# Optimization experiments

Hardware: AMD Instinct MI355X
Metric: run time of the kernel (lower is better)

The kernel has to match this reference:

```python
import jax, jax.numpy as jnp
import numpy as np

B, C_IN, L, NCLASS = 256, 6, 512, 10

def setup_inputs() -> dict:
    key = jax.random.key(0)
    ks = jax.random.split(key, 16)
    g = lambda k, shp, s=0.05: jax.random.normal(k, shp, dtype=jnp.float32) * s
    return {
        "x": jax.random.normal(ks[0], (B, C_IN, L), dtype=jnp.float32),
        "conv1_w": g(ks[1], (32, C_IN, 3)),
        "conv1_b": g(ks[2], (32,)),
        "bn1_g": jnp.ones((32,), jnp.float32),
        "bn1_b": jnp.zeros((32,), jnp.float32),
        "bn1_m": g(ks[3], (32,)),
        "bn1_v": jnp.abs(g(ks[4], (32,))) + 1.0,
        "conv2_w": g(ks[5], (64, 32, 3)),
        "conv2_b": g(ks[6], (64,)),
        "bn2_g": jnp.ones((64,), jnp.float32),
        "bn2_b": jnp.zeros((64,), jnp.float32),
        "bn2_m": g(ks[7], (64,)),
        "bn2_v": jnp.abs(g(ks[8], (64,))) + 1.0,
        "wq": g(ks[9], (64, 64)),
        "bq": g(ks[10], (64,)),
        "wk": g(ks[11], (64, 64)),
        "bk": g(ks[12], (64,)),
        "wv": g(ks[13], (64, 64)),
        "bv": g(ks[14], (64,)),
        "fc_w": g(ks[15], (NCLASS, 64)),
        "fc_b": jnp.zeros((NCLASS,), jnp.float32),
    }

def _conv1d(x, w, b):
    # x: [B, C, L], w: [O, C, 3], padding=1 -> same length
    y = jax.lax.conv_general_dilated(
        x, w, window_strides=(1,), padding=[(1, 1)],
        dimension_numbers=("NCH", "OIH", "NCH"))
    return y + b[None, :, None]

def _bn(x, g, b, m, v, eps=1e-5):
    # eval-mode BatchNorm1d over channel dim of [B, C, L]
    inv = g * jax.lax.rsqrt(v + eps)
    return x * inv[None, :, None] + (b - m * inv)[None, :, None]

def reference(x, conv1_w, conv1_b, bn1_g, bn1_b, bn1_m, bn1_v,
              conv2_w, conv2_b, bn2_g, bn2_b, bn2_m, bn2_v,
              wq, bq, wk, bk, wv, bv, fc_w, fc_b):
    h = jax.nn.relu(_bn(_conv1d(x, conv1_w, conv1_b), bn1_g, bn1_b, bn1_m, bn1_v))
    h = jax.nn.relu(_bn(_conv1d(h, conv2_w, conv2_b), bn2_g, bn2_b, bn2_m, bn2_v))
    h = h.transpose(0, 2, 1)                      # [B, L, 64]
    q = h @ wq.T + bq
    k = h @ wk.T + bk
    v = h @ wv.T + bv
    scores = jnp.einsum("bqd,bkd->bqk", q, k) / jnp.sqrt(jnp.float32(64.0))
    attn = jax.nn.softmax(scores, axis=-1)
    out = jnp.einsum("bqk,bkd->bqd", attn, v)     # [B, L, 64]
    pooled = out.mean(axis=1)                     # [B, 64]
    return pooled @ fc_w.T + fc_b                 # [B, n_class]
```

## Files before the change

### kernel.cpp

```cpp
#include <hip/hip_runtime.h>
#include <hip/hip_bf16.h>


#define NB 256
#define LL 512
#define CIN 6
#define NCLASS 10
#define SLAB 8192
#define QSC 0.18033688f

typedef __bf16 bf16x8 __attribute__((ext_vector_type(8)));
typedef float f32x4 __attribute__((ext_vector_type(4)));
typedef unsigned short us4 __attribute__((ext_vector_type(4)));
typedef unsigned short us8 __attribute__((ext_vector_type(8)));
typedef unsigned int u32x4 __attribute__((ext_vector_type(4)));

static __device__ __forceinline__ unsigned short f2b(float f) {
    __bf16 h = (__bf16)f;
    return __builtin_bit_cast(unsigned short, h);
}

__global__ __launch_bounds__(256) void prep_weights(
    const float* __restrict__ w1, const float* __restrict__ cb1,
    const float* __restrict__ g1, const float* __restrict__ be1,
    const float* __restrict__ m1, const float* __restrict__ v1,
    const float* __restrict__ w2, const float* __restrict__ cb2,
    const float* __restrict__ g2, const float* __restrict__ be2,
    const float* __restrict__ m2, const float* __restrict__ v2,
    const float* __restrict__ wq, const float* __restrict__ wk,
    const float* __restrict__ wv,
    unsigned short* __restrict__ w1p, float* __restrict__ b1f,
    unsigned short* __restrict__ w2p, float* __restrict__ b2f,
    unsigned short* __restrict__ wqp, unsigned short* __restrict__ wkp,
    unsigned short* __restrict__ wvp)
{
    const int tt = blockIdx.x * 256 + threadIdx.x;
    for (int idx = tt; idx < 1024; idx += 2048) {
        int c = idx >> 5, k = idx & 31;
        int dl = k >> 3, ci = k & 7;
        float inv = g1[c] * rsqrtf(v1[c] + 1e-5f);
        float val = (dl < 3 && ci < 6) ? w1[c * 18 + ci * 3 + dl] * inv : 0.f;
        w1p[idx] = f2b(val);
    }
    if (tt < 32) {
        float inv = g1[tt] * rsqrtf(v1[tt] + 1e-5f);
        b1f[tt] = be1[tt] + (cb1[tt] - m1[tt]) * inv;
    }
    for (int idx = tt; idx < 2048; idx += 2048) {
        int c2 = idx >> 5, ci = idx & 31;
        float inv = g2[c2] * rsqrtf(v2[c2] + 1e-5f);
        const float* wp = w2 + c2 * 96 + ci * 3;
        w2p[c2 * 96 +      ci] = f2b(wp[0] * inv);
        w2p[c2 * 96 + 32 + ci] = f2b(wp[1] * inv);
        w2p[c2 * 96 + 64 + ci] = f2b(wp[2] * inv);
    }
    if (tt >= 64 && tt < 128) {
        int c2 = tt - 64;
        float inv = g2[c2] * rsqrtf(v2[c2] + 1e-5f);
        b2f[c2] = be2[c2] + (cb2[c2] - m2[c2]) * inv;
    }
    for (int idx = tt; idx < 4096; idx += 2048) {
        int d = idx >> 6, k = idx & 63;
        int kc = k >> 5, quad = (k >> 3) & 3, e = k & 7;
        int ch = kc * 32 + (e >> 2) * 16 + quad * 4 + (e & 3);
        wqp[idx] = f2b(wq[d * 64 + ch] * QSC);
        wkp[idx] = f2b(wk[d * 64 + ch]);
        wvp[idx] = f2b(wv[d * 64 + ch]);
    }
}

__global__ __launch_bounds__(512, 2) void fused_all(
    const float* __restrict__ x,
    const unsigned short* __restrict__ w1p, const float* __restrict__ b1f,
    const unsigned short* __restrict__ w2p, const float* __restrict__ b2f,
    const unsigned short* __restrict__ wqp, const unsigned short* __restrict__ wkp,
    const unsigned short* __restrict__ wvp,
    const float* __restrict__ bq, const float* __restrict__ bk,
    const float* __restrict__ bvp,
    const float* __restrict__ fcw, const float* __restrict__ fcb,
    float* __restrict__ outp)
{
    const int b = blockIdx.x;
    const int t = threadIdx.x;
    const int w = t >> 6, lane = t & 63, quad = lane >> 4, lc = lane & 15;

    __shared__ __align__(16) char smem[16 * SLAB + 8192];
    unsigned short* xstage = (unsigned short*)(smem + 16 * SLAB);
    float* redw   = (float*)(smem + 16 * SLAB) + w * 64;
    float* pooled = (float*)(smem + 16 * SLAB + 4096);

    unsigned short* slab[2] = { (unsigned short*)(smem + (2 * w) * SLAB),
                                (unsigned short*)(smem + (2 * w + 1) * SLAB) };

    {
        us8 pk;
        #pragma unroll
        for (int ci = 0; ci < 6; ci++)
            pk[ci] = f2b(x[((size_t)b * CIN + ci) * LL + t]);
        pk[6] = 0; pk[7] = 0;
        *(us8*)&xstage[t * 8] = pk;
    }
    __syncthreads();

    {
        bf16x8 bW1[2];
        #pragma unroll
        for (int nt = 0; nt < 2; nt++)
            bW1[nt] = *(const bf16x8*)(w1p + (nt * 16 + lc) * 32 + quad * 8);
        f32x4 b1q[2];
        #pragma unroll
        for (int nt = 0; nt < 2; nt++)
            b1q[nt] = *(const f32x4*)&b1f[nt * 16 + quad * 4];
        #pragma unroll
        for (int sg = 0; sg < 2; sg++) {
            const int g = 2 * w + sg;
            unsigned short* h1sl = slab[sg];
            #pragma unroll
            for (int mt = 0; mt < 3; mt++) {
                int j = mt * 16 + lc;
                int P = g * 32 - 1 + j;
                int src = P + quad - 1;
                bool okx = (src >= 0) && (src < LL);
                int srcc = src < 0 ? 0 : (src > 511 ? 511 : src);
                u32x4 xv = *(const u32x4*)&xstage[srcc * 8];
                if (!okx) { xv[0] = 0u; xv[1] = 0u; xv[2] = 0u; xv[3] = 0u; }
                bf16x8 aX = __builtin_bit_cast(bf16x8, xv);
                bool pv = (P >= 0) && (P < LL);
                #pragma unroll
                for (int nt = 0; nt < 2; nt++) {
                    f32x4 z = {0.f, 0.f, 0.f, 0.f};
                    f32x4 h = __builtin_amdgcn_mfma_f32_16x16x32_bf16(bW1[nt], aX, z, 0, 0, 0);
                    us4 pk;
                    #pragma unroll
                    for (int r = 0; r < 4; r++) {
                        float y = h[r] + b1q[nt][r];
                        y = (pv && y > 0.f) ? y : 0.f;
                        pk[r] = f2b(y);
                    }
                    if (j < 34)
                        *(us4*)&h1sl[j * 40 + nt * 16 + quad * 4] = pk;
                }
            }
        }
    }

    bf16x8 bX[2][2][3];
    #pragma unroll
    for (int sg = 0; sg < 2; sg++)
        #pragma unroll
        for (int rt = 0; rt < 2; rt++)
            #pragma unroll
            for (int kc = 0; kc < 3; kc++)
                bX[sg][rt][kc] = *(const bf16x8*)&slab[sg][(rt * 16 + lc + kc) * 40 + quad * 8];

    f32x4 acc2[2][4][2];
    #pragma unroll
    for (int nt = 0; nt < 4; nt++) {
        bf16x8 aW0 = *(const bf16x8*)(w2p + (nt * 16 + lc) * 96 + quad * 8);
        bf16x8 aW1 = *(const bf16x8*)(w2p + (nt * 16 + lc) * 96 + 32 + quad * 8);
        bf16x8 aW2 = *(const bf16x8*)(w2p + (nt * 16 + lc) * 96 + 64 + quad * 8);
        #pragma unroll
        for (int sg = 0; sg < 2; sg++)
            #pragma unroll
            for (int rt = 0; rt < 2; rt++) {
                f32x4 a = {0.f, 0.f, 0.f, 0.f};
                a = __builtin_amdgcn_mfma_f32_16x16x32_bf16(aW0, bX[sg][rt][0], a, 0, 0, 0);
                a = __builtin_amdgcn_mfma_f32_16x16x32_bf16(aW1, bX[sg][rt][1], a, 0, 0, 0);
                acc2[sg][nt][rt] = __builtin_amdgcn_mfma_f32_16x16x32_bf16(aW2, bX[sg][rt][2], a, 0, 0, 0);
            }
    }

    bf16x8 aH[2][2][2];
    #pragma unroll
    for (int nt2 = 0; nt2 < 4; nt2++) {
        f32x4 bb2 = *(const f32x4*)&b2f[nt2 * 16 + quad * 4];
        #pragma unroll
        for (int sg = 0; sg < 2; sg++)
            #pragma unroll
            for (int rt = 0; rt < 2; rt++)
                #pragma unroll
                for (int reg = 0; reg < 4; reg++) {
                    float y = acc2[sg][nt2][rt][reg] + bb2[reg];
                    aH[sg][rt][nt2 >> 1][(nt2 & 1) * 4 + reg] = (__bf16)(y > 0.f ? y : 0.f);
                }
    }

    f32x4 bbq[4], bbk[4];
    #pragma unroll
    for (int nt = 0; nt < 4; nt++) {
        bbq[nt] = *(const f32x4*)&bq[nt * 16 + quad * 4];
        bbk[nt] = *(const f32x4*)&bk[nt * 16 + quad * 4];
    }

    bf16x8 aQ4[4][2];
    #pragma unroll
    for (int nt = 0; nt < 4; nt++) {
        bf16x8 aW0 = *(const bf16x8*)(wqp + (nt * 16 + lc) * 64 + quad * 8);
        bf16x8 aW1 = *(const bf16x8*)(wqp + (nt * 16 + lc) * 64 + 32 + quad * 8);
        #pragma unroll
        for (int sg = 0; sg < 2; sg++)
            #pragma unroll
            for (int rt = 0; rt < 2; rt++) {
                f32x4 a = {0.f, 0.f, 0.f, 0.f};
                a = __builtin_amdgcn_mfma_f32_16x16x32_bf16(aW0, aH[sg][rt][0], a, 0, 0, 0);
                a = __builtin_amdgcn_mfma_f32_16x16x32_bf16(aW1, aH[sg][rt][1], a, 0, 0, 0);
                #pragma unroll
                for (int reg = 0; reg < 4; reg++)
                    aQ4[sg * 2 + rt][nt >> 1][(nt & 1) * 4 + reg] =
                        (__bf16)(a[reg] + bbq[nt][reg] * QSC);
            }
    }

    #pragma unroll
    for (int kc = 0; kc < 2; kc++) {
        f32x4 Ck[2][2][2];
        #pragma unroll
        for (int j = 0; j < 2; j++) {
            int nt = kc * 2 + j;
            bf16x8 aW0 = *(const bf16x8*)(wkp + (nt * 16 + lc) * 64 + quad * 8);
            bf16x8 aW1 = *(const bf16x8*)(wkp + (nt * 16 + lc) * 64 + 32 + quad * 8);
            #pragma unroll
            for (int sg = 0; sg < 2; sg++)
                #pragma unroll
                for (int rt = 0; rt < 2; rt++) {
                    f32x4 a = {0.f, 0.f, 0.f, 0.f};
                    a = __builtin_amdgcn_mfma_f32_16x16x32_bf16(aW0, aH[sg][rt][0], a, 0, 0, 0);
                    Ck[j][sg][rt] = __builtin_amdgcn_mfma_f32_16x16x32_bf16(aW1, aH[sg][rt][1], a, 0, 0, 0);
                }
        }
        #pragma unroll
        for (int sg = 0; sg < 2; sg++)
            #pragma unroll
            for (int rt = 0; rt < 2; rt++) {
                us8 pk;
                #pragma unroll
                for (int e = 0; e < 8; e++) {
                    int j = e >> 2, reg = e & 3, nt = kc * 2 + j;
                    pk[e] = f2b(Ck[j][sg][rt][reg] + bbk[nt][reg]);
                }
                *(us8*)&slab[sg][((rt * 2 + kc) << 9) + lane * 8] = pk;
            }
    }

    #pragma unroll
    for (int nt = 0; nt < 4; nt++) {
        bf16x8 bW0 = *(const bf16x8*)(wvp + (nt * 16 + lc) * 64 + quad * 8);
        bf16x8 bW1 = *(const bf16x8*)(wvp + (nt * 16 + lc) * 64 + 32 + quad * 8);
        const float bvv = bvp[nt * 16 + lc];
        #pragma unroll
        for (int sg = 0; sg < 2; sg++) {
            f32x4 a0, a1;
            {
                f32x4 z = {0.f, 0.f, 0.f, 0.f};
                z = __builtin_amdgcn_mfma_f32_16x16x32_bf16(aH[sg][0][0], bW0, z, 0, 0, 0);
                a0 = __builtin_amdgcn_mfma_f32_16x16x32_bf16(aH[sg][0][1], bW1, z, 0, 0, 0);
            }
            {
                f32x4 z = {0.f, 0.f, 0.f, 0.f};
                z = __builtin_amdgcn_mfma_f32_16x16x32_bf16(aH[sg][1][0], bW0, z, 0, 0, 0);
                a1 = __builtin_amdgcn_mfma_f32_16x16x32_bf16(aH[sg][1][1], bW1, z, 0, 0, 0);
            }
            us8 pk;
            #pragma unroll
            for (int reg = 0; reg < 4; reg++) {
                pk[reg]     = f2b(a0[reg] + bvv);
                pk[4 + reg] = f2b(a1[reg] + bvv);
            }
            *(us8*)&slab[sg][2048 + nt * 512 + lane * 8] = pk;
        }
    }

    __syncthreads();

    f32x4 outacc[4][4];
    #pragma unroll
    for (int rt = 0; rt < 4; rt++)
        #pragma unroll
        for (int dt = 0; dt < 4; dt++) outacc[rt][dt] = (f32x4){0.f, 0.f, 0.f, 0.f};
    float den[4] = {0.f, 0.f, 0.f, 0.f};

    bf16x8 bK2[2][2];
    {
        const unsigned short* sK = (const unsigned short*)smem;
        #pragma unroll
        for (int nt = 0; nt < 2; nt++)
            #pragma unroll
            for (int kc = 0; kc < 2; kc++)
                bK2[nt][kc] = *(const bf16x8*)&sK[((nt * 2 + kc) << 9) + lane * 8];
    }
    f32x4 sv[2][4];
    #pragma unroll
    for (int nt = 0; nt < 2; nt++)
        #pragma unroll
        for (int rt = 0; rt < 4; rt++) {
            f32x4 z = {0.f, 0.f, 0.f, 0.f};
            z = __builtin_amdgcn_mfma_f32_16x16x32_bf16(bK2[nt][0], aQ4[rt][0], z, 0, 0, 0);
            sv[nt][rt] = __builtin_amdgcn_mfma_f32_16x16x32_bf16(bK2[nt][1], aQ4[rt][1], z, 0, 0, 0);
        }

    for (int cc = 0; cc < 16; cc++) {
        const unsigned short* sV = (const unsigned short*)(smem + cc * SLAB + 4096);
        bf16x8 bV[4];
        #pragma unroll
        for (int dt = 0; dt < 4; dt++)
            bV[dt] = *(const bf16x8*)&sV[dt * 512 + lane * 8];
        if (cc < 15) {
            const unsigned short* sKn = (const unsigned short*)(smem + (cc + 1) * SLAB);
            #pragma unroll
            for (int nt = 0; nt < 2; nt++)
                #pragma unroll
                for (int kc = 0; kc < 2; kc++)
                    bK2[nt][kc] = *(const bf16x8*)&sKn[((nt * 2 + kc) << 9) + lane * 8];
        }
        bf16x8 aP[4];
        #pragma unroll
        for (int rt = 0; rt < 4; rt++)
            #pragma unroll
            for (int nt = 0; nt < 2; nt++)
                #pragma unroll
                for (int reg = 0; reg < 4; reg++) {
                    float p = __builtin_amdgcn_exp2f(sv[nt][rt][reg]);
                    den[rt] += p;
                    aP[rt][nt * 4 + reg] = (__bf16)p;
                }
        __builtin_amdgcn_s_setprio(1);
        #pragma unroll
        for (int rt = 0; rt < 4; rt++)
            #pragma unroll
            for (int dt = 0; dt < 4; dt++)
                outacc[rt][dt] = __builtin_amdgcn_mfma_f32_16x16x32_bf16(aP[rt], bV[dt], outacc[rt][dt], 0, 0, 0);
        if (cc < 15) {
            #pragma unroll
            for (int nt = 0; nt < 2; nt++)
                #pragma unroll
                for (int rt = 0; rt < 4; rt++) {
                    f32x4 z = {0.f, 0.f, 0.f, 0.f};
                    z = __builtin_amdgcn_mfma_f32_16x16x32_bf16(bK2[nt][0], aQ4[rt][0], z, 0, 0, 0);
                    sv[nt][rt] = __builtin_amdgcn_mfma_f32_16x16x32_bf16(bK2[nt][1], aQ4[rt][1], z, 0, 0, 0);
                }
        }
        __builtin_amdgcn_s_setprio(0);
    }

    float rden[4][4];
    #pragma unroll
    for (int rt = 0; rt < 4; rt++) {
        float d2 = den[rt];
        d2 += __shfl_xor(d2, 16);
        d2 += __shfl_xor(d2, 32);
        d2 = 1.0f / d2;
        #pragma unroll
        for (int reg = 0; reg < 4; reg++)
            rden[rt][reg] = __shfl(d2, quad * 4 + reg);
    }
    #pragma unroll
    for (int dt = 0; dt < 4; dt++) {
        float ps = 0.f;
        #pragma unroll
        for (int rt = 0; rt < 4; rt++)
            #pragma unroll
            for (int reg = 0; reg < 4; reg++)
                ps += outacc[rt][dt][reg] * rden[rt][reg];
        ps += __shfl_xor(ps, 16);
        ps += __shfl_xor(ps, 32);
        if (quad == 0) redw[dt * 16 + lc] = ps;
    }
    __syncthreads();
    if (t < 64) {
        float s = 0.f;
        #pragma unroll
        for (int ww = 0; ww < 8; ww++)
            s += *(const float*)(smem + 16 * SLAB + ww * 256 + t * 4);
        pooled[t] = s * (1.0f / 512.0f);
    }
    __syncthreads();
    if (t < NCLASS) {
        float acc = fcb[t];
        #pragma unroll
        for (int d = 0; d < 64; d++) acc += pooled[d] * fcw[t * 64 + d];
        outp[b * NCLASS + t] = acc;
    }
}

extern "C" void kernel_launch(void* const* d_in, const int* in_sizes, int n_in,
                              void* d_out, int out_size, void* d_ws, size_t ws_size,
                              hipStream_t stream)
{
    const float* x   = (const float*)d_in[0];
    const float* w1  = (const float*)d_in[1];
    const float* cb1 = (const float*)d_in[2];
    const float* g1  = (const float*)d_in[3];
    const float* be1 = (const float*)d_in[4];
    const float* m1  = (const float*)d_in[5];
    const float* v1  = (const float*)d_in[6];
    const float* w2  = (const float*)d_in[7];
    const float* cb2 = (const float*)d_in[8];
    const float* g2  = (const float*)d_in[9];
    const float* be2 = (const float*)d_in[10];
    const float* m2  = (const float*)d_in[11];
    const float* v2  = (const float*)d_in[12];
    const float* wq  = (const float*)d_in[13];
    const float* bq  = (const float*)d_in[14];
    const float* wk  = (const float*)d_in[15];
    const float* bk  = (const float*)d_in[16];
    const float* wv  = (const float*)d_in[17];
    const float* bv  = (const float*)d_in[18];
    const float* fcw = (const float*)d_in[19];
    const float* fcb = (const float*)d_in[20];
    float* out = (float*)d_out;

    char* ws = (char*)d_ws;
    unsigned short* w1p = (unsigned short*)(ws);
    float*          b1f = (float*)(ws + 2048u);
    float*          b2f = (float*)(ws + 2176u);
    unsigned short* w2p = (unsigned short*)(ws + 2432u);
    unsigned short* wqp = (unsigned short*)(ws + 14720u);
    unsigned short* wkp = (unsigned short*)(ws + 22912u);
    unsigned short* wvp = (unsigned short*)(ws + 31104u);

    prep_weights<<<dim3(8), 256, 0, stream>>>(w1, cb1, g1, be1, m1, v1,
                                              w2, cb2, g2, be2, m2, v2,
                                              wq, wk, wv,
                                              w1p, b1f, w2p, b2f, wqp, wkp, wvp);
    fused_all<<<dim3(NB), 512, 0, stream>>>(x, w1p, b1f, w2p, b2f,
                                            wqp, wkp, wvp,
                                            bq, bk, bv, fcw, fcb, out);
}
```

Before: 119.3 us.

## Software-pipeline attention loop with double-buffered K/V registers and early score MFMAs

Restructures the attention key-chunk loop into a two-stage software pipeline. K fragments are prefetched two chunks ahead and V fragments one chunk ahead into double-buffered registers. Next-chunk QK score MFMAs are issued before the current chunk's exp/PV work, so LDS reads and MFMA latency overlap the exp2 computation. The loop is fully unrolled. This roughly doubles register use for K, V and score fragments, which may lower occupancy or cause spills.

New measurement: 118.7 us. Within noise of the previous version (-0.5%).

```diff
diff --git a/kernel.cpp b/kernel.cpp
--- a/kernel.cpp
+++ b/kernel.cpp
@@ -279,38 +279,61 @@
         for (int dt = 0; dt < 4; dt++) outacc[rt][dt] = (f32x4){0.f, 0.f, 0.f, 0.f};
     float den[4] = {0.f, 0.f, 0.f, 0.f};
 
-    bf16x8 bK2[2][2];
+    bf16x8 bK2[2][2][2];
+    bf16x8 bV2[2][4];
+    f32x4 sv2[2][2][4];
     {
-        const unsigned short* sK = (const unsigned short*)smem;
+        const unsigned short* sK0 = (const unsigned short*)smem;
+        const unsigned short* sK1 = (const unsigned short*)(smem + SLAB);
+        const unsigned short* sV0 = (const unsigned short*)(smem + 4096);
         #pragma unroll
         for (int nt = 0; nt < 2; nt++)
             #pragma unroll
-            for (int kc = 0; kc < 2; kc++)
-                bK2[nt][kc] = *(const bf16x8*)&sK[((nt * 2 + kc) << 9) + lane * 8];
-    }
-    f32x4 sv[2][4];
-    #pragma unroll
-    for (int nt = 0; nt < 2; nt++)
-        #pragma unroll
-        for (int rt = 0; rt < 4; rt++) {
-            f32x4 z = {0.f, 0.f, 0.f, 0.f};
-            z = __builtin_amdgcn_mfma_f32_16x16x32_bf16(bK2[nt][0], aQ4[rt][0], z, 0, 0, 0);
-            sv[nt][rt] = __builtin_amdgcn_mfma_f32_16x16x32_bf16(bK2[nt][1], aQ4[rt][1], z, 0, 0, 0);
-        }
-
+            for (int kc = 0; kc < 2; kc++) {
+                bK2[0][nt][kc] = *(const bf16x8*)&sK0[((nt * 2 + kc) << 9) + lane * 8];
+                bK2[1][nt][kc] = *(const bf16x8*)&sK1[((nt * 2 + kc) << 9) + lane * 8];
+            }
+        #pragma unroll
+        for (int dt = 0; dt < 4; dt++)
+            bV2[0][dt] = *(const bf16x8*)&sV0[dt * 512 + lane * 8];
+        #pragma unroll
+        for (int nt = 0; nt < 2; nt++)
+            #pragma unroll
+            for (int rt = 0; rt < 4; rt++) {
+                f32x4 z = {0.f, 0.f, 0.f, 0.f};
+                z = __builtin_amdgcn_mfma_f32_16x16x32_bf16(bK2[0][nt][0], aQ4[rt][0], z, 0, 0, 0);
+                sv2[0][nt][rt] = __builtin_amdgcn_mfma_f32_16x16x32_bf16(bK2[0][nt][1], aQ4[rt][1], z, 0, 0, 0);
+            }
+    }
+
+    #pragma unroll
     for (int cc = 0; cc < 16; cc++) {
-        const unsigned short* sV = (const unsigned short*)(smem + cc * SLAB + 4096);
-        bf16x8 bV[4];
-        #pragma unroll
-        for (int dt = 0; dt < 4; dt++)
-            bV[dt] = *(const bf16x8*)&sV[dt * 512 + lane * 8];
+        const int cur = cc & 1, nxt = (cc + 1) & 1;
+        if (cc < 14) {
+            const unsigned short* sKn = (const unsigned short*)(smem + (cc + 2) * SLAB);
+            #pragma unroll
+            for (int nt = 0; nt < 2; nt++)
+                #pragma unroll
+                for (int kc = 0; kc < 2; kc++)
+                    bK2[cur][nt][kc] = *(const bf16x8*)&sKn[((nt * 2 + kc) << 9) + lane * 8];
+        }
         if (cc < 15) {
-            const unsigned short* sKn = (const unsigned short*)(smem + (cc + 1) * SLAB);
+            const unsigned short* sVn = (const unsigned short*)(smem + (cc + 1) * SLAB + 4096);
+            #pragma unroll
+            for (int dt = 0; dt < 4; dt++)
+                bV2[nxt][dt] = *(const bf16x8*)&sVn[dt * 512 + lane * 8];
+        }
+        if (cc < 15) {
+            __builtin_amdgcn_s_setprio(1);
             #pragma unroll
             for (int nt = 0; nt < 2; nt++)
                 #pragma unroll
-                for (int kc = 0; kc < 2; kc++)
-                    bK2[nt][kc] = *(const bf16x8*)&sKn[((nt * 2 + kc) << 9) + lane * 8];
+                for (int rt = 0; rt < 4; rt++) {
+                    f32x4 z = {0.f, 0.f, 0.f, 0.f};
+                    z = __builtin_amdgcn_mfma_f32_16x16x32_bf16(bK2[nxt][nt][0], aQ4[rt][0], z, 0, 0, 0);
+                    sv2[nxt][nt][rt] = __builtin_amdgcn_mfma_f32_16x16x32_bf16(bK2[nxt][nt][1], aQ4[rt][1], z, 0, 0, 0);
+                }
+            __builtin_amdgcn_s_setprio(0);
         }
         bf16x8 aP[4];
         #pragma unroll
@@ -319,7 +342,7 @@
             for (int nt = 0; nt < 2; nt++)
                 #pragma unroll
                 for (int reg = 0; reg < 4; reg++) {
-                    float p = __builtin_amdgcn_exp2f(sv[nt][rt][reg]);
+                    float p = __builtin_amdgcn_exp2f(sv2[cur][nt][rt][reg]);
                     den[rt] += p;
                     aP[rt][nt * 4 + reg] = (__bf16)p;
                 }
@@ -328,17 +351,7 @@
         for (int rt = 0; rt < 4; rt++)
             #pragma unroll
             for (int dt = 0; dt < 4; dt++)
-                outacc[rt][dt] = __builtin_amdgcn_mfma_f32_16x16x32_bf16(aP[rt], bV[dt], outacc[rt][dt], 0, 0, 0);
-        if (cc < 15) {
-            #pragma unroll
-            for (int nt = 0; nt < 2; nt++)
-                #pragma unroll
-                for (int rt = 0; rt < 4; rt++) {
-                    f32x4 z = {0.f, 0.f, 0.f, 0.f};
-                    z = __builtin_amdgcn_mfma_f32_16x16x32_bf16(bK2[nt][0], aQ4[rt][0], z, 0, 0, 0);
-                    sv[nt][rt] = __builtin_amdgcn_mfma_f32_16x16x32_bf16(bK2[nt][1], aQ4[rt][1], z, 0, 0, 0);
-                }
-        }
+                outacc[rt][dt] = __builtin_amdgcn_mfma_f32_16x16x32_bf16(aP[rt], bV2[cur][dt], outacc[rt][dt], 0, 0, 0);
         __builtin_amdgcn_s_setprio(0);
     }
 
```
